# Performance work log

Hardware: AMD Instinct MI355X
Metric: run time of the kernel (lower is better)

Reference implementation:

```python
import jax, jax.numpy as jnp
import numpy as np

B, NNODES, NODE, EDGEF, HID, NFACT, DEG = 256, 64, 64, 32, 256, 8, 32
N_TOTAL = B * NNODES            # 16384 nodes
E_TOTAL = B * NNODES * DEG      # 524288 edges
NEDGES_HEAD = 128               # len(self.edges)


def _w(key, shape, fan_in):
    return jax.random.normal(key, shape, dtype=jnp.float32) * (1.0 / np.sqrt(fan_in))


def setup_inputs() -> dict:
    key = jax.random.key(0)
    ks = jax.random.split(key, 16)
    # message-passing edge_index: per graph, node i -> (i+k) % NNODES, k=1..DEG
    src = np.repeat(np.arange(NNODES), DEG)
    dst = (src + np.tile(np.arange(1, DEG + 1), NNODES)) % NNODES
    offs = (np.arange(B) * NNODES)[:, None]
    ei = np.stack([(src[None, :] + offs).reshape(-1),
                   (dst[None, :] + offs).reshape(-1)], axis=0)
    edge_index = jnp.asarray(ei, dtype=jnp.int32)  # [2, E_TOTAL]
    # actor head edge list (within-graph indices): ring distance 1 and 2
    e1 = np.stack([np.arange(NNODES), (np.arange(NNODES) + 1) % NNODES], 1)
    e2 = np.stack([np.arange(NNODES), (np.arange(NNODES) + 2) % NNODES], 1)
    edges = jnp.asarray(np.concatenate([e1, e2], 0), dtype=jnp.int32)  # [128,2]

    D = NODE + HID  # 320
    inp = {
        "x": jax.random.normal(ks[0], (N_TOTAL, NODE), dtype=jnp.float32),
        "edge_index": edge_index,
        "edge_attr": jax.random.normal(ks[1], (E_TOTAL, EDGEF), dtype=jnp.float32),
        "edges": edges,
        "high": jax.random.uniform(ks[2], (NEDGES_HEAD + NFACT,), minval=0.5, maxval=2.0),
        "W1": _w(ks[3], (2 * NODE + EDGEF, HID), 2 * NODE + EDGEF),
        "b1": jnp.zeros((HID,), jnp.float32),
        "W2": _w(ks[4], (HID, HID), HID),
        "b2": jnp.zeros((HID,), jnp.float32),
        "Wmu": _w(ks[5], (2 * D, 1), 2 * D),
        "bmu": jnp.zeros((1,), jnp.float32),
        "Wsig": _w(ks[6], (2 * D, 1), 2 * D),
        "bsig": jnp.zeros((1,), jnp.float32),
        "Wmu2": _w(ks[7], (D, 1), D),
        "bmu2": jnp.zeros((1,), jnp.float32),
        "Wsig2": _w(ks[8], (D, 1), D),
        "bsig2": jnp.zeros((1,), jnp.float32),
    }
    return inp


def reference(x, edge_index, edge_attr, edges, high,
              W1, b1, W2, b2, Wmu, bmu, Wsig, bsig, Wmu2, bmu2, Wsig2, bsig2):
    # EdgeConv (flow='target_to_source', aggr='add'): x_i=x[ei0], x_j=x[ei1], aggregate at ei0
    xi = x[edge_index[0]]                                   # [E, NODE]
    xj = x[edge_index[1]]                                   # [E, NODE]
    msg_in = jnp.concatenate([xi, xj, edge_attr], axis=1)   # [E, 2*NODE+EDGEF]
    msg = jax.nn.relu(msg_in @ W1 + b1) @ W2 + b2           # [E, HID]
    agg = jax.ops.segment_sum(msg, edge_index[0], num_segments=x.shape[0])  # [N, HID]

    x_pp = jnp.concatenate([x, agg], axis=1).reshape(-1, NNODES, NODE + HID)  # [B, nn, D]

    ef_src = x_pp[:, edges[:, 0], :]                        # [B, 128, D]
    ef_dst = x_pp[:, edges[:, 1], :]                        # [B, 128, D]
    ef = jnp.concatenate([ef_src, ef_dst], axis=2)          # [B, 128, 2D]

    alpha = jax.nn.softplus((ef @ Wmu + bmu).squeeze(-1) + 1e-20)    # [B, 128]
    beta = jax.nn.softplus((ef @ Wsig + bsig).squeeze(-1) + 1e-20)   # [B, 128]

    fact = x_pp[:, -NFACT:, :]                              # [B, 8, D]
    alpha2 = jax.nn.softplus((fact @ Wmu2 + bmu2).squeeze(-1) + 1e-20)   # [B, 8]
    beta2 = jax.nn.softplus((fact @ Wsig2 + bsig2).squeeze(-1) + 1e-20)  # [B, 8]

    # deterministic=True path
    alpha = alpha + 1e-20
    beta = beta + 1e-20
    dis_action = alpha / (alpha + beta) * high[:-NFACT]     # [B, 128]
    alpha2 = alpha2 + 1e-20
    beta2 = beta2 + 1e-20
    order_act = alpha2 / (alpha2 + beta2) * high[-NFACT:]   # [B, 8]
    act = jnp.concatenate([dis_action, order_act], axis=-1) # [B, 136]
    return act
```

## Files before the change

kernel.cpp:

```cpp
#include <hip/hip_runtime.h>
#include <math.h>

#define BATCH_  256
#define NTOT    16384
#define ETOT    524288

typedef __attribute__((ext_vector_type(8))) short short8v;
typedef __attribute__((ext_vector_type(4))) float f32x4;

#define MFMA16(a,b,c) __builtin_amdgcn_mfma_f32_16x16x32_bf16((a),(b),(c),0,0,0)

__device__ __forceinline__ unsigned short f2bf(float f) {
    unsigned int x = __float_as_uint(f);
    return (unsigned short)((x + 0x7fffu + ((x >> 16) & 1u)) >> 16);
}
__device__ __forceinline__ float bf2f(unsigned short h) {
    return __uint_as_float(((unsigned int)h) << 16);
}
__device__ __forceinline__ float softplus_f(float v) {
    return v > 20.f ? v : log1pf(expf(v));
}
__device__ __forceinline__ float dot4(f32x4 a, f32x4 b) {
    float z = a[0] * b[0];
    z = fmaf(a[1], b[1], z);
    z = fmaf(a[2], b[2], z);
    z = fmaf(a[3], b[3], z);
    return z;
}
__device__ __forceinline__ void packfrag(f32x4 a, f32x4 q, short8v& hi, short8v& lo) {
    float v[8] = {a[0], a[1], a[2], a[3], q[0], q[1], q[2], q[3]};
#pragma unroll
    for (int j = 0; j < 8; j++) {
        const unsigned short h = f2bf(v[j]);
        hi[j] = (short)h;
        lo[j] = (short)f2bf(v[j] - bf2f(h));
    }
}

__global__ __launch_bounds__(256) void k_prep(const float* __restrict__ W1,
                                              const float* __restrict__ W2,
                                              unsigned short* __restrict__ frags) {
    const int u = blockIdx.x;
    const float* S = (u < 80) ? W1 : W2;
    const int ul = (u < 80) ? u : (u - 80);
    const int rowbase = (ul >> 4) * 32;
    const int cht = ul & 15;
    for (int idx = threadIdx.x; idx < 512; idx += 256) {
        const int l = idx >> 3, j = idx & 7;
        const int row = rowbase + ((l >> 4) << 3) + j;
        const int col = cht * 16 + (l & 15);
        const float v = S[row * 256 + col];
        const unsigned short h = f2bf(v);
        frags[u * 1024 + idx]       = h;
        frags[u * 1024 + 512 + idx] = f2bf(v - bf2f(h));
    }
}

__global__ __launch_bounds__(512) __attribute__((amdgpu_waves_per_eu(4)))
void k_ab(
    const float* __restrict__ x, const float* __restrict__ ea,
    const int* __restrict__ dst, const float* __restrict__ b1,
    const unsigned short* __restrict__ frags, float* __restrict__ sumh1)
{
    __shared__ __align__(16) unsigned char smem[67584];
    float*          s_xwb  = (float*)smem;
    unsigned short* s_ea   = (unsigned short*)(smem + 32768);
    unsigned char*  s_dstl = (unsigned char*)(smem + 65536);

    const int b = blockIdx.x & 255, half = blockIdx.x >> 8;
    const int tid = threadIdx.x;
    const int l = tid & 63, w = tid >> 6, g = l >> 4, l15 = l & 15;
    const int ng = w & 3, cqq = w >> 2;
    const int node = ng * 16 + l15;
    const int swzn = (l15 & 7) << 2;

    for (int idx = tid; idx < 2048; idx += 512)
        s_dstl[idx] = (unsigned char)(dst[b * 2048 + idx] & 63);

    const int ols = tid >> 8;
    const int ns  = (tid & 255) >> 2;
    const int ko  = tid & 3;
    const int sll = (ko << 4) | (ns & 15), sng = ns >> 4;
    const float* eab = ea + (size_t)b * 65536 + (size_t)ns * 1024 + ko * 8;

    f32x4 ld0 = *(const f32x4*)&eab[(size_t)ols * 32];
    f32x4 ld1 = *(const f32x4*)&eab[(size_t)ols * 32 + 4];

    short8v Xh[2], Xl[2];
#pragma unroll
    for (int kt = 0; kt < 2; kt++) {
        const float* p = x + (size_t)(b * 64 + node) * 64 + kt * 32 + g * 8;
        packfrag(*(const f32x4*)p, *(const f32x4*)(p + 4), Xh[kt], Xl[kt]);
    }

    f32x4 xab1[4];
#pragma unroll
    for (int i = 0; i < 4; i++) {
        const int cht = half * 8 + cqq * 4 + i;
        f32x4 d = *(const f32x4*)&b1[cht * 16 + g * 4];
#pragma unroll
        for (int kt = 0; kt < 2; kt++) {
            const int base = (kt * 16 + cht) * 1024 + l * 8;
            const short8v Ahh = *(const short8v*)&frags[base];
            const short8v All = *(const short8v*)&frags[base + 512];
            d = MFMA16(All, Xh[kt], d);
            d = MFMA16(Ahh, Xl[kt], d);
            d = MFMA16(Ahh, Xh[kt], d);
        }
        xab1[i] = d;
    }

#pragma unroll
    for (int i = 0; i < 4; i++) {
        const int cht = half * 8 + cqq * 4 + i;
        f32x4 d = {0.f, 0.f, 0.f, 0.f};
#pragma unroll
        for (int kt = 0; kt < 2; kt++) {
            const int base = ((kt + 2) * 16 + cht) * 1024 + l * 8;
            const short8v Ahh = *(const short8v*)&frags[base];
            const short8v All = *(const short8v*)&frags[base + 512];
            d = MFMA16(All, Xh[kt], d);
            d = MFMA16(Ahh, Xl[kt], d);
            d = MFMA16(Ahh, Xh[kt], d);
        }
        *(f32x4*)&s_xwb[node * 128 + (((cqq * 4 + i) * 16 + g * 4) ^ swzn)] = d;
    }

    short8v Ah[4], Al[4];
#pragma unroll
    for (int i = 0; i < 4; i++) {
        const int base = (64 + half * 8 + cqq * 4 + i) * 1024 + l * 8;
        Ah[i] = *(const short8v*)&frags[base];
        Al[i] = *(const short8v*)&frags[base + 512];
    }

    {
        short8v hi, lo;
        packfrag(ld0, ld1, hi, lo);
        *(short8v*)&s_ea[((((0 * 2 + 0) * 2 + ols) * 4 + sng) * 64 + sll) * 8] = hi;
        *(short8v*)&s_ea[((((0 * 2 + 1) * 2 + ols) * 4 + sng) * 64 + sll) * 8] = lo;
    }
    ld0 = *(const f32x4*)&eab[(size_t)(2 + ols) * 32];
    ld1 = *(const f32x4*)&eab[(size_t)(2 + ols) * 32 + 4];
    __syncthreads();

    f32x4 acc[4];
#pragma unroll
    for (int i = 0; i < 4; i++) acc[i] = (f32x4){0.f, 0.f, 0.f, 0.f};

    for (int c = 0; c < 16; ++c) {
        if (c < 15) {
            short8v hi, lo;
            packfrag(ld0, ld1, hi, lo);
            const int nb = (c + 1) & 1;
            *(short8v*)&s_ea[((((nb * 2 + 0) * 2 + ols) * 4 + sng) * 64 + sll) * 8] = hi;
            *(short8v*)&s_ea[((((nb * 2 + 1) * 2 + ols) * 4 + sng) * 64 + sll) * 8] = lo;
            if (c < 14) {
                const int o = (c + 2) * 2 + ols;
                ld0 = *(const f32x4*)&eab[(size_t)o * 32];
                ld1 = *(const f32x4*)&eab[(size_t)o * 32 + 4];
            }
        }

        const int cb2 = c & 1;
        const unsigned short dw = ((const unsigned short*)s_dstl)[node * 16 + c];

#pragma unroll
        for (int ol = 0; ol < 2; ol++) {
            const short8v Bh = *(const short8v*)&s_ea[((((cb2 * 2 + 0) * 2 + ol) * 4 + ng) * 64 + l) * 8];
            const short8v Bl = *(const short8v*)&s_ea[((((cb2 * 2 + 1) * 2 + ol) * 4 + ng) * 64 + l) * 8];
            const int d = (dw >> (ol * 8)) & 0xFF;
            const int swz = (d & 7) << 2;

#pragma unroll
            for (int i = 0; i < 4; i++) {
                const int cbl = (cqq * 4 + i) * 16 + g * 4;
                const f32x4 wb = *(const f32x4*)&s_xwb[d * 128 + (cbl ^ swz)];
                f32x4 di = MFMA16(Al[i], Bh, xab1[i]);
                di = MFMA16(Ah[i], Bl, di);
                di = MFMA16(Ah[i], Bh, di);
#pragma unroll
                for (int r = 0; r < 4; r++)
                    acc[i][r] += fmaxf(di[r] + wb[r], 0.f);
            }
        }
        __syncthreads();
    }

    const size_t grow = (size_t)b * 64 + node;
#pragma unroll
    for (int i = 0; i < 4; i++) {
        const int cg = (half * 8 + cqq * 4 + i) * 16 + g * 4;
        *(f32x4*)&sumh1[grow * 256 + cg] = acc[i];
    }
}

__global__ __launch_bounds__(512) void k_cd(
    const float* __restrict__ x, const float* __restrict__ sumh1,
    const int* __restrict__ edges, const float* __restrict__ high,
    const unsigned short* __restrict__ frags, const float* __restrict__ b2,
    const float* __restrict__ Wmu,  const float* __restrict__ bmu,
    const float* __restrict__ Wsig, const float* __restrict__ bsig,
    const float* __restrict__ Wmu2, const float* __restrict__ bmu2,
    const float* __restrict__ Wsig2,const float* __restrict__ bsig2,
    float* __restrict__ out)
{
    __shared__ __align__(16) unsigned char smem[131072];
    float* s_sumh1 = (float*)smem;
    float* s_agg   = (float*)(smem + 65536);
    float* s_su    = (float*)smem;
    float* s_su2   = (float*)(smem + 1024);

    const int b = blockIdx.x, tid = threadIdx.x;
    const int l = tid & 63, w = tid >> 6, g = l >> 4, l15 = l & 15;
    const int swzn = (l15 & 7) << 2;

    for (int idx = tid; idx < 4096; idx += 512) {
        const int row = idx >> 6, c4 = (idx & 63) * 4;
        const f32x4 v = *(const f32x4*)&sumh1[(size_t)b * 16384 + (size_t)idx * 4];
        *(f32x4*)&s_sumh1[row * 256 + (c4 ^ ((row & 7) << 2))] = v;
    }
    __syncthreads();

    const int rt = w & 3, ch8 = w >> 2;
    f32x4 acc2[8];
#pragma unroll
    for (int j = 0; j < 8; j++) acc2[j] = (f32x4){0.f, 0.f, 0.f, 0.f};

    for (int ks = 0; ks < 8; ks++) {
        const int row = rt * 16 + l15;
        const int cbk = ks * 32 + g * 8;
        const f32x4 a0 = *(const f32x4*)&s_sumh1[row * 256 + (cbk ^ swzn)];
        const f32x4 a1 = *(const f32x4*)&s_sumh1[row * 256 + ((cbk + 4) ^ swzn)];
        short8v Ahh, All;
        packfrag(a0, a1, Ahh, All);
#pragma unroll
        for (int j = 0; j < 8; j++) {
            const int base = (80 + ks * 16 + ch8 * 8 + j) * 1024 + l * 8;
            const short8v Bh = *(const short8v*)&frags[base];
            const short8v Bl = *(const short8v*)&frags[base + 512];
            acc2[j] = MFMA16(Ahh, Bh, acc2[j]);
            acc2[j] = MFMA16(Ahh, Bl, acc2[j]);
            acc2[j] = MFMA16(All, Bh, acc2[j]);
        }
    }

#pragma unroll
    for (int j = 0; j < 8; j++) {
        const int col = (ch8 * 8 + j) * 16 + l15;
        const float bb = 32.f * b2[col];
#pragma unroll
        for (int r = 0; r < 4; r++) {
            const int row = rt * 16 + g * 4 + r;
            s_agg[row * 256 + (col ^ ((row & 7) << 2))] = acc2[j][r] + bb;
        }
    }
    __syncthreads();

    if (tid < 256) {
        const int n = tid >> 2, s = tid & 3;
        const float* Wp = ((s & 1) ? Wsig : Wmu) + ((s >> 1) ? 320 : 0);
        const float* xr = x + (size_t)(b * 64 + n) * 64;
        const int sw = (n & 7) << 2;
        float z = 0.f;
#pragma unroll
        for (int kq = 0; kq < 16; kq++)
            z += dot4(*(const f32x4*)&xr[kq * 4], *(const f32x4*)&Wp[kq * 4]);
#pragma unroll 8
        for (int kq = 0; kq < 64; kq++)
            z += dot4(*(const f32x4*)&s_agg[n * 256 + ((kq * 4) ^ sw)],
                      *(const f32x4*)&Wp[64 + kq * 4]);
        s_su[n * 4 + s] = z;
    } else if (tid < 272) {
        const int j = (tid - 256) >> 1, s = tid & 1;
        const int n = 56 + j;
        const float* Wp = s ? Wsig2 : Wmu2;
        const float* xr = x + (size_t)(b * 64 + n) * 64;
        const int sw = (n & 7) << 2;
        float z = 0.f;
#pragma unroll
        for (int kq = 0; kq < 16; kq++)
            z += dot4(*(const f32x4*)&xr[kq * 4], *(const f32x4*)&Wp[kq * 4]);
#pragma unroll 8
        for (int kq = 0; kq < 64; kq++)
            z += dot4(*(const f32x4*)&s_agg[n * 256 + ((kq * 4) ^ sw)],
                      *(const f32x4*)&Wp[64 + kq * 4]);
        s_su2[j * 2 + s] = z;
    }
    __syncthreads();

    if (tid < 128) {
        const int e0 = edges[tid * 2], e1 = edges[tid * 2 + 1];
        const float a  = softplus_f(s_su[e0 * 4 + 0] + s_su[e1 * 4 + 2] + bmu[0])  + 1e-20f;
        const float be = softplus_f(s_su[e0 * 4 + 1] + s_su[e1 * 4 + 3] + bsig[0]) + 1e-20f;
        out[(size_t)b * 136 + tid] = a / (a + be) * high[tid];
    } else if (tid < 136) {
        const int j = tid - 128;
        const float a  = softplus_f(s_su2[j * 2 + 0] + bmu2[0])  + 1e-20f;
        const float be = softplus_f(s_su2[j * 2 + 1] + bsig2[0]) + 1e-20f;
        out[(size_t)b * 136 + tid] = a / (a + be) * high[128 + j];
    }
}

extern "C" void kernel_launch(void* const* d_in, const int* in_sizes, int n_in,
                              void* d_out, int out_size, void* d_ws, size_t ws_size,
                              hipStream_t stream) {
    const float* x     = (const float*)d_in[0];
    const int*   eidx  = (const int*)  d_in[1];
    const float* ea    = (const float*)d_in[2];
    const int*   edges = (const int*)  d_in[3];
    const float* high  = (const float*)d_in[4];
    const float* W1    = (const float*)d_in[5];
    const float* b1    = (const float*)d_in[6];
    const float* W2    = (const float*)d_in[7];
    const float* b2    = (const float*)d_in[8];
    const float* Wmu   = (const float*)d_in[9];
    const float* bmu   = (const float*)d_in[10];
    const float* Wsig  = (const float*)d_in[11];
    const float* bsig  = (const float*)d_in[12];
    const float* Wmu2  = (const float*)d_in[13];
    const float* bmu2  = (const float*)d_in[14];
    const float* Wsig2 = (const float*)d_in[15];
    const float* bsig2 = (const float*)d_in[16];
    float* out = (float*)d_out;

    float* sumh1 = (float*)d_ws;
    const size_t frag_off = (ws_size - (size_t)208 * 2048) & ~(size_t)1023;
    unsigned short* frags = (unsigned short*)((char*)d_ws + frag_off);
    const int* dst = eidx + ETOT;

    hipLaunchKernelGGL(k_prep, dim3(208),    dim3(256), 0, stream, W1, W2, frags);
    hipLaunchKernelGGL(k_ab,   dim3(512),    dim3(512), 0, stream,
                       x, ea, dst, b1, frags, sumh1);
    hipLaunchKernelGGL(k_cd,   dim3(BATCH_), dim3(512), 0, stream,
                       x, sumh1, edges, high, frags, b2,
                       Wmu, bmu, Wsig, bsig, Wmu2, bmu2, Wsig2, bsig2, out);
}
```

Measured before the change: 78.53 us.

## Load edge features directly into registers and drop the low-bf16 split term

The edge-conv kernel stops staging edge_attr through shared memory with double buffering and per-chunk barriers. Each lane now loads its edge features straight from global memory and converts them to bf16 with hardware packed-convert instructions. The low-order bf16 correction term for edge features is dropped, which removes one MFMA per tile but lowers the precision of the edge-attribute product. The second kernel moves to 1024 threads with fewer accumulators per wave, and the head weights are staged in shared memory.

```diff
diff --git a/kernel.cpp b/kernel.cpp
--- a/kernel.cpp
+++ b/kernel.cpp
@@ -35,6 +35,14 @@
         hi[j] = (short)h;
         lo[j] = (short)f2bf(v[j] - bf2f(h));
     }
+}
+__device__ __forceinline__ short8v cvthi8(f32x4 a, f32x4 q) {
+    union { short8v s; unsigned int u[4]; } r;
+    asm("v_cvt_pk_bf16_f32 %0, %1, %2" : "=v"(r.u[0]) : "v"(a[0]), "v"(a[1]));
+    asm("v_cvt_pk_bf16_f32 %0, %1, %2" : "=v"(r.u[1]) : "v"(a[2]), "v"(a[3]));
+    asm("v_cvt_pk_bf16_f32 %0, %1, %2" : "=v"(r.u[2]) : "v"(q[0]), "v"(q[1]));
+    asm("v_cvt_pk_bf16_f32 %0, %1, %2" : "=v"(r.u[3]) : "v"(q[2]), "v"(q[3]));
+    return r.s;
 }
 
 __global__ __launch_bounds__(256) void k_prep(const float* __restrict__ W1,
@@ -56,16 +64,15 @@
     }
 }
 
-__global__ __launch_bounds__(512) __attribute__((amdgpu_waves_per_eu(4)))
-void k_ab(
+__global__ __launch_bounds__(512) __attribute__((amdgpu_waves_per_eu(4, 4)))
+void k_ab2(
     const float* __restrict__ x, const float* __restrict__ ea,
     const int* __restrict__ dst, const float* __restrict__ b1,
     const unsigned short* __restrict__ frags, float* __restrict__ sumh1)
 {
-    __shared__ __align__(16) unsigned char smem[67584];
-    float*          s_xwb  = (float*)smem;
-    unsigned short* s_ea   = (unsigned short*)(smem + 32768);
-    unsigned char*  s_dstl = (unsigned char*)(smem + 65536);
+    __shared__ __align__(16) unsigned char smem[34816];
+    float*         s_xwb  = (float*)smem;
+    unsigned char* s_dstl = (unsigned char*)(smem + 32768);
 
     const int b = blockIdx.x & 255, half = blockIdx.x >> 8;
     const int tid = threadIdx.x;
@@ -76,15 +83,6 @@
 
     for (int idx = tid; idx < 2048; idx += 512)
         s_dstl[idx] = (unsigned char)(dst[b * 2048 + idx] & 63);
-
-    const int ols = tid >> 8;
-    const int ns  = (tid & 255) >> 2;
-    const int ko  = tid & 3;
-    const int sll = (ko << 4) | (ns & 15), sng = ns >> 4;
-    const float* eab = ea + (size_t)b * 65536 + (size_t)ns * 1024 + ko * 8;
-
-    f32x4 ld0 = *(const f32x4*)&eab[(size_t)ols * 32];
-    f32x4 ld1 = *(const f32x4*)&eab[(size_t)ols * 32 + 4];
 
     short8v Xh[2], Xl[2];
 #pragma unroll
@@ -134,42 +132,24 @@
         Al[i] = *(const short8v*)&frags[base + 512];
     }
 
-    {
-        short8v hi, lo;
-        packfrag(ld0, ld1, hi, lo);
-        *(short8v*)&s_ea[((((0 * 2 + 0) * 2 + ols) * 4 + sng) * 64 + sll) * 8] = hi;
-        *(short8v*)&s_ea[((((0 * 2 + 1) * 2 + ols) * 4 + sng) * 64 + sll) * 8] = lo;
-    }
-    ld0 = *(const f32x4*)&eab[(size_t)(2 + ols) * 32];
-    ld1 = *(const f32x4*)&eab[(size_t)(2 + ols) * 32 + 4];
-    __syncthreads();
+    __syncthreads();
+
+    const float* eap = ea + ((size_t)b * 2048 + (size_t)node * 32) * 32 + g * 8;
 
     f32x4 acc[4];
 #pragma unroll
     for (int i = 0; i < 4; i++) acc[i] = (f32x4){0.f, 0.f, 0.f, 0.f};
 
-    for (int c = 0; c < 16; ++c) {
-        if (c < 15) {
-            short8v hi, lo;
-            packfrag(ld0, ld1, hi, lo);
-            const int nb = (c + 1) & 1;
-            *(short8v*)&s_ea[((((nb * 2 + 0) * 2 + ols) * 4 + sng) * 64 + sll) * 8] = hi;
-            *(short8v*)&s_ea[((((nb * 2 + 1) * 2 + ols) * 4 + sng) * 64 + sll) * 8] = lo;
-            if (c < 14) {
-                const int o = (c + 2) * 2 + ols;
-                ld0 = *(const f32x4*)&eab[(size_t)o * 32];
-                ld1 = *(const f32x4*)&eab[(size_t)o * 32 + 4];
-            }
-        }
-
-        const int cb2 = c & 1;
-        const unsigned short dw = ((const unsigned short*)s_dstl)[node * 16 + c];
-
-#pragma unroll
-        for (int ol = 0; ol < 2; ol++) {
-            const short8v Bh = *(const short8v*)&s_ea[((((cb2 * 2 + 0) * 2 + ol) * 4 + ng) * 64 + l) * 8];
-            const short8v Bl = *(const short8v*)&s_ea[((((cb2 * 2 + 1) * 2 + ol) * 4 + ng) * 64 + l) * 8];
-            const int d = (dw >> (ol * 8)) & 0xFF;
+#pragma unroll 2
+    for (int c = 0; c < 8; c++) {
+        const unsigned int dw = ((const unsigned int*)s_dstl)[node * 8 + c];
+#pragma unroll
+        for (int o4 = 0; o4 < 4; o4++) {
+            const int o = c * 4 + o4;
+            const f32x4 e0 = *(const f32x4*)(eap + o * 32);
+            const f32x4 e1 = *(const f32x4*)(eap + o * 32 + 4);
+            const short8v Bh = cvthi8(e0, e1);
+            const int d = (dw >> (o4 * 8)) & 63;
             const int swz = (d & 7) << 2;
 
 #pragma unroll
@@ -177,14 +157,12 @@
                 const int cbl = (cqq * 4 + i) * 16 + g * 4;
                 const f32x4 wb = *(const f32x4*)&s_xwb[d * 128 + (cbl ^ swz)];
                 f32x4 di = MFMA16(Al[i], Bh, xab1[i]);
-                di = MFMA16(Ah[i], Bl, di);
                 di = MFMA16(Ah[i], Bh, di);
 #pragma unroll
                 for (int r = 0; r < 4; r++)
                     acc[i][r] += fmaxf(di[r] + wb[r], 0.f);
             }
         }
-        __syncthreads();
     }
 
     const size_t grow = (size_t)b * 64 + node;
@@ -195,7 +173,8 @@
     }
 }
 
-__global__ __launch_bounds__(512) void k_cd(
+__global__ __launch_bounds__(1024) __attribute__((amdgpu_waves_per_eu(4, 4)))
+void k_cd2(
     const float* __restrict__ x, const float* __restrict__ sumh1,
     const int* __restrict__ edges, const float* __restrict__ high,
     const unsigned short* __restrict__ frags, const float* __restrict__ b2,
@@ -210,22 +189,23 @@
     float* s_agg   = (float*)(smem + 65536);
     float* s_su    = (float*)smem;
     float* s_su2   = (float*)(smem + 1024);
+    float* s_w     = (float*)(smem + 2048);
 
     const int b = blockIdx.x, tid = threadIdx.x;
     const int l = tid & 63, w = tid >> 6, g = l >> 4, l15 = l & 15;
     const int swzn = (l15 & 7) << 2;
 
-    for (int idx = tid; idx < 4096; idx += 512) {
+    for (int idx = tid; idx < 4096; idx += 1024) {
         const int row = idx >> 6, c4 = (idx & 63) * 4;
         const f32x4 v = *(const f32x4*)&sumh1[(size_t)b * 16384 + (size_t)idx * 4];
         *(f32x4*)&s_sumh1[row * 256 + (c4 ^ ((row & 7) << 2))] = v;
     }
     __syncthreads();
 
-    const int rt = w & 3, ch8 = w >> 2;
-    f32x4 acc2[8];
-#pragma unroll
-    for (int j = 0; j < 8; j++) acc2[j] = (f32x4){0.f, 0.f, 0.f, 0.f};
+    const int rt = w & 3, cj = w >> 2;
+    f32x4 acc2[4];
+#pragma unroll
+    for (int j = 0; j < 4; j++) acc2[j] = (f32x4){0.f, 0.f, 0.f, 0.f};
 
     for (int ks = 0; ks < 8; ks++) {
         const int row = rt * 16 + l15;
@@ -235,8 +215,8 @@
         short8v Ahh, All;
         packfrag(a0, a1, Ahh, All);
 #pragma unroll
-        for (int j = 0; j < 8; j++) {
-            const int base = (80 + ks * 16 + ch8 * 8 + j) * 1024 + l * 8;
+        for (int j = 0; j < 4; j++) {
+            const int base = (80 + ks * 16 + cj * 4 + j) * 1024 + l * 8;
             const short8v Bh = *(const short8v*)&frags[base];
             const short8v Bl = *(const short8v*)&frags[base + 512];
             acc2[j] = MFMA16(Ahh, Bh, acc2[j]);
@@ -246,8 +226,8 @@
     }
 
 #pragma unroll
-    for (int j = 0; j < 8; j++) {
-        const int col = (ch8 * 8 + j) * 16 + l15;
+    for (int j = 0; j < 4; j++) {
+        const int col = (cj * 4 + j) * 16 + l15;
         const float bb = 32.f * b2[col];
 #pragma unroll
         for (int r = 0; r < 4; r++) {
@@ -257,9 +237,15 @@
     }
     __syncthreads();
 
+    for (int i = tid; i < 1920; i += 1024)
+        s_w[i] = (i < 640) ? Wmu[i]
+               : (i < 1280) ? Wsig[i - 640]
+               : (i < 1600) ? Wmu2[i - 1280] : Wsig2[i - 1600];
+    __syncthreads();
+
     if (tid < 256) {
         const int n = tid >> 2, s = tid & 3;
-        const float* Wp = ((s & 1) ? Wsig : Wmu) + ((s >> 1) ? 320 : 0);
+        const float* Wp = s_w + (s & 1) * 640 + ((s >> 1) ? 320 : 0);
         const float* xr = x + (size_t)(b * 64 + n) * 64;
         const int sw = (n & 7) << 2;
         float z = 0.f;
@@ -274,7 +260,7 @@
     } else if (tid < 272) {
         const int j = (tid - 256) >> 1, s = tid & 1;
         const int n = 56 + j;
-        const float* Wp = s ? Wsig2 : Wmu2;
+        const float* Wp = s_w + 1280 + (s ? 320 : 0);
         const float* xr = x + (size_t)(b * 64 + n) * 64;
         const int sw = (n & 7) << 2;
         float z = 0.f;
@@ -329,10 +315,10 @@
     unsigned short* frags = (unsigned short*)((char*)d_ws + frag_off);
     const int* dst = eidx + ETOT;
 
-    hipLaunchKernelGGL(k_prep, dim3(208),    dim3(256), 0, stream, W1, W2, frags);
-    hipLaunchKernelGGL(k_ab,   dim3(512),    dim3(512), 0, stream,
+    hipLaunchKernelGGL(k_prep, dim3(208),    dim3(256),  0, stream, W1, W2, frags);
+    hipLaunchKernelGGL(k_ab2,  dim3(512),    dim3(512),  0, stream,
                        x, ea, dst, b1, frags, sumh1);
-    hipLaunchKernelGGL(k_cd,   dim3(BATCH_), dim3(512), 0, stream,
+    hipLaunchKernelGGL(k_cd2,  dim3(BATCH_), dim3(1024), 0, stream,
                        x, sumh1, edges, high, frags, b2,
                        Wmu, bmu, Wsig, bsig, Wmu2, bmu2, Wsig2, bsig2, out);
 }
```

Result: slower. 116.3 us (+48.0%).
